# Performance work log

Measured on AMD Instinct MI355X. Metric: run time of the kernel, lower is better.

The kernel has to match this reference:

```python
import jax, jax.numpy as jnp
import numpy as np

N, S, C, E = 32768, 32768, 1024, 16384   # nodes, subgraph-node entries, clusters (=B*P), coarsen edges
F, D, B, P, NC = 64, 64, 16, 64, 10      # feat dim, hidden, graphs, patches per graph, classes


def setup_inputs():
    key = jax.random.key(0)
    ks = list(jax.random.split(key, 24))
    p = lambda k, shp: jax.random.normal(k, shp, dtype=jnp.float32) * 0.05
    z = lambda n: jnp.zeros((n,), jnp.float32)
    return {
        "x": jax.random.normal(ks[0], (N, F), dtype=jnp.float32),
        "subgraphs_nodes_mapper": jax.random.randint(ks[1], (S,), 0, N, dtype=jnp.int32),
        "subgraphs_batch": jnp.sort(jax.random.randint(ks[2], (S,), 0, C, dtype=jnp.int32)),
        "subgraphs_batch_row": jax.random.randint(ks[3], (E,), 0, C, dtype=jnp.int32),
        "subgraphs_batch_col": jax.random.randint(ks[4], (E,), 0, C, dtype=jnp.int32),
        "coarsen_edge_attr": jax.random.uniform(ks[5], (E,), dtype=jnp.float32),
        "W_in1": p(ks[6], (F, D)), "b_in1": z(D),
        "W_in2": p(ks[7], (D, D)), "b_in2": z(D),
        "W_pre1": p(ks[8], (D, D)), "b_pre1": z(D),
        "W_pre2": p(ks[9], (D, D)), "b_pre2": z(D),
        "W_post1": p(ks[10], (D, D)), "b_post1": z(D),
        "W_post2": p(ks[11], (D, D)), "b_post2": z(D),
        "W_K": p(ks[12], (D, D)), "b_K": z(D),
        "W_V": p(ks[13], (D, D)), "b_V": z(D),
        "alpha_beta": jax.random.normal(ks[14], (2,), dtype=jnp.float32),
        "W_c1": p(ks[15], (D, D // 2)), "b_c1": z(D // 2),
        "W_c2": p(ks[16], (D // 2, NC)), "b_c2": z(NC),
    }


def reference(x, subgraphs_nodes_mapper, subgraphs_batch, subgraphs_batch_row,
              subgraphs_batch_col, coarsen_edge_attr,
              W_in1, b_in1, W_in2, b_in2, W_pre1, b_pre1, W_pre2, b_pre2,
              W_post1, b_post1, W_post2, b_post2, W_K, b_K, W_V, b_V,
              alpha_beta, W_c1, b_c1, W_c2, b_c2):
    seg_sum = lambda v, idx: jax.ops.segment_sum(v, idx, num_segments=C)
    # input transform MLP (use_gnn=False path)
    h = jax.nn.relu(x @ W_in1 + b_in1)
    h = jax.nn.relu(h @ W_in2 + b_in2)
    sx = h[subgraphs_nodes_mapper]                        # [S, D] irregular gather
    b = subgraphs_batch
    row, col = subgraphs_batch_row, subgraphs_batch_col
    # bincount-based symmetric degree normalization of coarsened edge weights
    deg = seg_sum(coarsen_edge_attr, row)                 # [C]
    dinv = jnp.where(deg > 0, deg ** -0.5, 0.0)
    ea = dinv[row] * coarsen_edge_attr * dinv[col]        # [E]
    # Q path: pre-deepset -> scatter sum -> post-deepset
    Q = jax.nn.relu(sx @ W_pre1 + b_pre1) @ W_pre2 + b_pre2
    Qs = seg_sum(Q, b)
    Qs = jax.nn.relu(Qs @ W_post1 + b_post1) @ W_post2 + b_post2  # [C, D]
    # K / V paths
    K = sx @ W_K + b_K                                    # [S, D]
    cnt = jnp.maximum(seg_sum(jnp.ones((S,), sx.dtype), b), 1.0)
    Ks = seg_sum(K, b) / cnt[:, None]                     # scatter-mean [C, D]
    V = sx @ W_V + b_V                                    # [S, D]
    # relu kernelization
    Qk, Kk, Ksk = jax.nn.relu(Qs), jax.nn.relu(K), jax.nn.relu(Ks)
    ab = jax.nn.softmax(alpha_beta)
    sa, sb = ab[0] ** -0.5, ab[1] ** -0.5
    ck = jnp.concatenate([sa * Ksk[b], sb * Kk], axis=-1)   # [S, 2D]
    cq = jnp.concatenate([sa * Qk, sb * Qk], axis=-1)       # [C, 2D] (diffQ=False)
    ck_s = seg_sum(ck, b)                                   # [C, 2D]
    M = ck[:, :, None] * V[:, None, :]                      # [S, 2D, D] per-entry outer product
    Ms = seg_sum(M, b)                                      # [C, 2D, D]
    # Double_Level_MessageProp / KeyProp on coarsened graph: out[c] = sum_e ea_e * x[row_e] at col_e
    Ms = seg_sum(ea[:, None, None] * Ms[row], col)
    ck_s = seg_sum(ea[:, None] * ck_s[row], col)
    H = jnp.einsum('ci,cij->cj', cq, Ms)                    # [C, D]
    den = jnp.sum(cq * ck_s, axis=-1, keepdims=True) + 1e-6
    out = H / den                                           # [C, D]
    g = out.reshape(B, P, D).mean(axis=1)                   # mean readout over patches
    logits = jax.nn.relu(g @ W_c1 + b_c1) @ W_c2 + b_c2     # [B, NC]
    return logits
```

## Files before the change

### kernel.cpp

```cpp
#include <hip/hip_runtime.h>
#include <math.h>

constexpr int NN = 32768;
constexpr int SS = 32768;
constexpr int CC = 1024;
constexpr int EE = 16384;
constexpr int BB = 16;
constexpr int PP = 64;
constexpr int NC = 10;

__device__ __forceinline__ float rdlane(float v, int l) {
    return __int_as_float(__builtin_amdgcn_readlane(__float_as_int(v), l));
}

__global__ __launch_bounds__(256) void k_zero(float* __restrict__ zbase)
{
    int i = blockIdx.x * 256 + threadIdx.x;
    *(float4*)(zbase + (size_t)i * 4) = make_float4(0.f, 0.f, 0.f, 0.f);
}

#define TS 68

__device__ __forceinline__ void gemm64(const float* A, const float* W,
                                       const float* __restrict__ bias,
                                       int r0, int c0, float acc[4][4])
{
#pragma unroll
    for (int dc = 0; dc < 4; ++dc) {
        float bv = bias[c0 + dc];
        acc[0][dc] = bv; acc[1][dc] = bv; acc[2][dc] = bv; acc[3][dc] = bv;
    }
#pragma unroll 16
    for (int k = 0; k < 64; ++k) {
        float4 av = *(const float4*)(A + k * TS + r0);
        float4 wv = *(const float4*)(W + k * TS + c0);
        acc[0][0] = fmaf(av.x, wv.x, acc[0][0]); acc[0][1] = fmaf(av.x, wv.y, acc[0][1]);
        acc[0][2] = fmaf(av.x, wv.z, acc[0][2]); acc[0][3] = fmaf(av.x, wv.w, acc[0][3]);
        acc[1][0] = fmaf(av.y, wv.x, acc[1][0]); acc[1][1] = fmaf(av.y, wv.y, acc[1][1]);
        acc[1][2] = fmaf(av.y, wv.z, acc[1][2]); acc[1][3] = fmaf(av.y, wv.w, acc[1][3]);
        acc[2][0] = fmaf(av.z, wv.x, acc[2][0]); acc[2][1] = fmaf(av.z, wv.y, acc[2][1]);
        acc[2][2] = fmaf(av.z, wv.z, acc[2][2]); acc[2][3] = fmaf(av.z, wv.w, acc[2][3]);
        acc[3][0] = fmaf(av.w, wv.x, acc[3][0]); acc[3][1] = fmaf(av.w, wv.y, acc[3][1]);
        acc[3][2] = fmaf(av.w, wv.z, acc[3][2]); acc[3][3] = fmaf(av.w, wv.w, acc[3][3]);
    }
}

__device__ __forceinline__ void gemm64x2(const float* A, const float* W1_, const float* W2_,
                                         const float* __restrict__ bias1,
                                         const float* __restrict__ bias2,
                                         int r0, int c0, float acc1[4][4], float acc2[4][4])
{
#pragma unroll
    for (int dc = 0; dc < 4; ++dc) {
        float bv1 = bias1[c0 + dc], bv2 = bias2[c0 + dc];
#pragma unroll
        for (int dr = 0; dr < 4; ++dr) { acc1[dr][dc] = bv1; acc2[dr][dc] = bv2; }
    }
#pragma unroll 8
    for (int k = 0; k < 64; ++k) {
        float4 av = *(const float4*)(A + k * TS + r0);
        float4 w1 = *(const float4*)(W1_ + k * TS + c0);
        float4 w2 = *(const float4*)(W2_ + k * TS + c0);
        float ar[4] = {av.x, av.y, av.z, av.w};
        float u1[4] = {w1.x, w1.y, w1.z, w1.w};
        float u2[4] = {w2.x, w2.y, w2.z, w2.w};
#pragma unroll
        for (int dr = 0; dr < 4; ++dr)
#pragma unroll
            for (int dc = 0; dc < 4; ++dc) {
                acc1[dr][dc] = fmaf(ar[dr], u1[dc], acc1[dr][dc]);
                acc2[dr][dc] = fmaf(ar[dr], u2[dc], acc2[dr][dc]);
            }
    }
}

__device__ __forceinline__ void stageW(float* dst, const float* __restrict__ src, int tid)
{
#pragma unroll
    for (int t = 0; t < 16; ++t) {
        int idx = tid + t * 256;
        dst[(idx >> 6) * TS + (idx & 63)] = src[idx];
    }
}

__device__ __forceinline__ void outT_relu(float* dst, int r0, int c0, float acc[4][4])
{
#pragma unroll
    for (int dc = 0; dc < 4; ++dc) {
        *(float4*)(dst + (c0 + dc) * TS + r0) =
            make_float4(fmaxf(acc[0][dc], 0.f), fmaxf(acc[1][dc], 0.f),
                        fmaxf(acc[2][dc], 0.f), fmaxf(acc[3][dc], 0.f));
    }
}

__device__ __forceinline__ void outG2(float* __restrict__ dst, size_t rowbase, int ld,
                                      int off, int r0, int c0, float acc[4][4], bool dorelu)
{
#pragma unroll
    for (int dr = 0; dr < 4; ++dr) {
        float4 v = make_float4(acc[dr][0], acc[dr][1], acc[dr][2], acc[dr][3]);
        if (dorelu) {
            v.x = fmaxf(v.x, 0.f); v.y = fmaxf(v.y, 0.f);
            v.z = fmaxf(v.z, 0.f); v.w = fmaxf(v.w, 0.f);
        }
        *(float4*)(dst + (rowbase + r0 + dr) * ld + off + c0) = v;
    }
}

__global__ __launch_bounds__(256) void k_node(
    const float* __restrict__ x,
    const float* __restrict__ W1, const float* __restrict__ b1,
    const float* __restrict__ W2, const float* __restrict__ b2,
    const float* __restrict__ Wp1, const float* __restrict__ bp1,
    const float* __restrict__ WK, const float* __restrict__ bK,
    const float* __restrict__ WV, const float* __restrict__ bV,
    float* __restrict__ u, float* __restrict__ KV)
{
    __shared__ __align__(16) float bufA[64 * TS];
    __shared__ __align__(16) float bufB[64 * TS];
    __shared__ __align__(16) float wlds[64 * TS];
    int tid = threadIdx.x;
    int tx = tid & 15, ty = tid >> 4;
    int r0 = ty * 4, c0 = tx * 4;
    size_t rowbase = (size_t)blockIdx.x * 64;
    const float* xb = x + rowbase * 64;
#pragma unroll
    for (int t = 0; t < 16; ++t) {
        int idx = tid + t * 256;
        bufA[(idx & 63) * TS + (idx >> 6)] = xb[idx];
    }
    stageW(wlds, W1, tid);
    __syncthreads();
    float acc[4][4];
    gemm64(bufA, wlds, b1, r0, c0, acc);
    outT_relu(bufB, r0, c0, acc);
    __syncthreads();
    stageW(wlds, W2, tid);
    __syncthreads();
    gemm64(bufB, wlds, b2, r0, c0, acc);
    outT_relu(bufA, r0, c0, acc);
    __syncthreads();
    stageW(wlds, Wp1, tid);
    __syncthreads();
    gemm64(bufA, wlds, bp1, r0, c0, acc);
    outG2(u, rowbase, 64, 0, r0, c0, acc, true);
    __syncthreads();
    stageW(wlds, WK, tid);
    stageW(bufB, WV, tid);
    __syncthreads();
    float accV[4][4];
    gemm64x2(bufA, wlds, bufB, bK, bV, r0, c0, acc, accV);
    outG2(KV, rowbase, 128, 0, r0, c0, acc, false);
    outG2(KV, rowbase, 128, 64, r0, c0, accV, false);
}

__global__ void k_prep1(const int* __restrict__ row, const float* __restrict__ attr,
                        float* __restrict__ deg, int* __restrict__ rowcnt, int E)
{
    int e = blockIdx.x * 256 + threadIdx.x;
    if (e < E) {
        int r = row[e];
        atomicAdd(&deg[r], attr[e]);
        atomicAdd(&rowcnt[r], 1);
    }
}

__global__ __launch_bounds__(1024) void k_scan(
    const int* __restrict__ rowcnt, int* __restrict__ rowptr, int* __restrict__ rowfill,
    const int* __restrict__ batch, int* __restrict__ segoff)
{
    __shared__ int buf[1024];
    int tid = threadIdx.x;
    int v = rowcnt[tid];
    buf[tid] = v;
    __syncthreads();
    for (int off = 1; off < 1024; off <<= 1) {
        int t = (tid >= off) ? buf[tid - off] : 0;
        __syncthreads();
        buf[tid] += t;
        __syncthreads();
    }
    int incl = buf[tid];
    if (tid == 0) rowptr[0] = 0;
    rowptr[tid + 1] = incl;
    rowfill[tid] = incl - v;
    int lo = 0, hi = SS;
    while (lo < hi) { int mid = (lo + hi) >> 1; if (batch[mid] < tid) lo = mid + 1; else hi = mid; }
    segoff[tid] = lo;
    if (tid == 0) segoff[CC] = SS;
}

__global__ void k_prep2(const int* __restrict__ row, const int* __restrict__ col,
                        const float* __restrict__ attr, const float* __restrict__ deg,
                        int* __restrict__ rowfill, int* __restrict__ colS,
                        float* __restrict__ eawS, int E)
{
    int e = blockIdx.x * 256 + threadIdx.x;
    if (e < E) {
        int r = row[e], c = col[e];
        float dr = deg[r], dc = deg[c];
        float ir = dr > 0.f ? 1.f / sqrtf(dr) : 0.f;
        float ic = dc > 0.f ? 1.f / sqrtf(dc) : 0.f;
        int pos = atomicAdd(&rowfill[r], 1);
        colS[pos] = c;
        eawS[pos] = ir * attr[e] * ic;
    }
}

#define KSTR 72

__global__ __launch_bounds__(256, 4) void k_msb(
    const float* __restrict__ u, const float* __restrict__ KV,
    const int* __restrict__ mapper, const int* __restrict__ segoff,
    const float* __restrict__ Wp2, const float* __restrict__ bp2,
    const float* __restrict__ Wpo1, const float* __restrict__ bpo1,
    const float* __restrict__ Wpo2, const float* __restrict__ bpo2,
    float* __restrict__ Msb, float* __restrict__ Qk, float* __restrict__ Ksk,
    float* __restrict__ Krsum, float* __restrict__ Vsum, float* __restrict__ Lf)
{
    __shared__ __align__(16) float Kr[32 * KSTR];
    __shared__ __align__(16) float Vb[32 * KSTR];
    __shared__ int map_lds[32];
    __shared__ float sums[256];
    __shared__ float redu0[64], redu1[64], redu2[64];
    int c = blockIdx.x;
    int tid = threadIdx.x, j = tid & 63, g = tid >> 6;
    int tx = tid & 15, ty = tid >> 4;
    int r0 = ty * 4, c0 = tx * 4;
    int s0 = segoff[c], s1 = segoff[c + 1];
    sums[tid] = 0.f;
    float acc[4][4];
#pragma unroll
    for (int a = 0; a < 4; ++a)
#pragma unroll
        for (int b = 0; b < 4; ++b) acc[a][b] = 0.f;
    float qs = 0.f, ks = 0.f, krs = 0.f, vs = 0.f;
    __syncthreads();
    for (int sb = s0; sb < s1; sb += 32) {
        int clen = min(32, s1 - sb);
        __syncthreads();
        if (tid < clen) map_lds[tid] = mapper[sb + tid];
        __syncthreads();
        for (int p = tid; p < clen * 32; p += 256) {
            int e = p >> 5, q = p & 31;
            int m = map_lds[e];
            float4 v = *(const float4*)(KV + (size_t)m * 128 + q * 4);
            float* dst = (q < 16) ? &Kr[e * KSTR + q * 4] : &Vb[e * KSTR + (q - 16) * 4];
            *(float4*)dst = v;
        }
        __syncthreads();
#pragma unroll 4
        for (int s = 0; s < clen; ++s) {
            float4 a4 = *(const float4*)(&Kr[s * KSTR + r0]);
            float4 b4 = *(const float4*)(&Vb[s * KSTR + c0]);
            float ar0 = fmaxf(a4.x, 0.f), ar1 = fmaxf(a4.y, 0.f);
            float ar2 = fmaxf(a4.z, 0.f), ar3 = fmaxf(a4.w, 0.f);
            acc[0][0] = fmaf(ar0, b4.x, acc[0][0]); acc[0][1] = fmaf(ar0, b4.y, acc[0][1]);
            acc[0][2] = fmaf(ar0, b4.z, acc[0][2]); acc[0][3] = fmaf(ar0, b4.w, acc[0][3]);
            acc[1][0] = fmaf(ar1, b4.x, acc[1][0]); acc[1][1] = fmaf(ar1, b4.y, acc[1][1]);
            acc[1][2] = fmaf(ar1, b4.z, acc[1][2]); acc[1][3] = fmaf(ar1, b4.w, acc[1][3]);
            acc[2][0] = fmaf(ar2, b4.x, acc[2][0]); acc[2][1] = fmaf(ar2, b4.y, acc[2][1]);
            acc[2][2] = fmaf(ar2, b4.z, acc[2][2]); acc[2][3] = fmaf(ar2, b4.w, acc[2][3]);
            acc[3][0] = fmaf(ar3, b4.x, acc[3][0]); acc[3][1] = fmaf(ar3, b4.y, acc[3][1]);
            acc[3][2] = fmaf(ar3, b4.z, acc[3][2]); acc[3][3] = fmaf(ar3, b4.w, acc[3][3]);
        }
        for (int s = g; s < clen; s += 4) {
            float kv = Kr[s * KSTR + j];
            ks += kv;
            krs += fmaxf(kv, 0.f);
            vs += Vb[s * KSTR + j];
            qs += u[(size_t)map_lds[s] * 64 + j];
        }
    }
    atomicAdd(&sums[j], qs);
    atomicAdd(&sums[64 + j], ks);
    atomicAdd(&sums[128 + j], krs);
    atomicAdd(&sums[192 + j], vs);
    size_t mb = (size_t)c * 4096;
#pragma unroll
    for (int a = 0; a < 4; ++a)
        *(float4*)(Msb + mb + (size_t)(r0 + a) * 64 + c0) =
            make_float4(acc[a][0], acc[a][1], acc[a][2], acc[a][3]);
    int L = s1 - s0;
    if (tid < 64) {
        redu0[tid] = (float)L * bp2[tid];
        redu1[tid] = bpo1[tid];
        redu2[tid] = bpo2[tid];
    }
    __syncthreads();
    float qsv = sums[j];
    float Lm = (float)(L > 0 ? L : 1);
    if (g == 0) {
        Ksk[c * 64 + j] = fmaxf(sums[64 + j] / Lm, 0.f);
        Krsum[c * 64 + j] = sums[128 + j];
        Vsum[c * 64 + j] = sums[192 + j];
        if (j == 0) Lf[c] = (float)L;
    }
    float p = 0.f;
#pragma unroll
    for (int t = 0; t < 16; ++t) {
        int i = g * 16 + t;
        p = fmaf(rdlane(qsv, i), Wp2[i * 64 + j], p);
    }
    atomicAdd(&redu0[j], p);
    __syncthreads();
    float q2 = redu0[j];
    p = 0.f;
#pragma unroll
    for (int t = 0; t < 16; ++t) {
        int i = g * 16 + t;
        p = fmaf(rdlane(q2, i), Wpo1[i * 64 + j], p);
    }
    atomicAdd(&redu1[j], p);
    __syncthreads();
    float tt = fmaxf(redu1[j], 0.f);
    p = 0.f;
#pragma unroll
    for (int t = 0; t < 16; ++t) {
        int i = g * 16 + t;
        p = fmaf(rdlane(tt, i), Wpo2[i * 64 + j], p);
    }
    atomicAdd(&redu2[j], p);
    __syncthreads();
    if (tid < 64) Qk[c * 64 + tid] = fmaxf(redu2[tid], 0.f);
}

#define MSTR 68

__global__ __launch_bounds__(256, 4) void k_edges(
    const float* __restrict__ Msb, const float* __restrict__ Qk,
    const float* __restrict__ Ksk, const float* __restrict__ Krsum,
    const float* __restrict__ Vsum, const float* __restrict__ Lf,
    const float* __restrict__ eawS, const int* __restrict__ colS,
    const int* __restrict__ rowptr, const float* __restrict__ ab,
    float* __restrict__ H, float* __restrict__ den)
{
    __shared__ __align__(16) float msb[64 * MSTR];
    int r = blockIdx.x;
    int e0 = rowptr[r], e1 = rowptr[r + 1];
    if (e0 == e1) return;
    int tid = threadIdx.x, j = tid & 63, g = tid >> 6;
    size_t mb = (size_t)r * 4096;
    for (int p = tid; p < 1024; p += 256) {
        float4 v = *(const float4*)(Msb + mb + (size_t)p * 4);
        int i = p >> 4, j0 = (p & 15) * 4;
        *(float4*)(&msb[i * MSTR + j0]) = v;
    }
    float kskj = Ksk[r * 64 + j];
    float krj  = Krsum[r * 64 + j];
    float vsj  = Vsum[r * 64 + j];
    float Lr   = Lf[r];
    float a0 = ab[0], a1 = ab[1];
    float sa2 = 1.f + expf(a1 - a0);
    float sb2 = 1.f + expf(a0 - a1);
    __syncthreads();
    int idx = e0 + g;
    if (idx >= e1) return;
    int c = colS[idx];
    float w = eawS[idx];
    float qv = Qk[c * 64 + j];
    while (true) {
        int cc = c; float wc = w, qc = qv;
        int nidx = idx + 4;
        if (nidx < e1) {
            c = colS[nidx];
            w = eawS[nidx];
            qv = Qk[c * 64 + j];
        }
        float wj0 = 0.f, wj1 = 0.f, wj2 = 0.f, wj3 = 0.f;
#pragma unroll
        for (int t = 0; t < 16; ++t) {
            wj0 = fmaf(rdlane(qc, 4 * t + 0), msb[(4 * t + 0) * MSTR + j], wj0);
            wj1 = fmaf(rdlane(qc, 4 * t + 1), msb[(4 * t + 1) * MSTR + j], wj1);
            wj2 = fmaf(rdlane(qc, 4 * t + 2), msb[(4 * t + 2) * MSTR + j], wj2);
            wj3 = fmaf(rdlane(qc, 4 * t + 3), msb[(4 * t + 3) * MSTR + j], wj3);
        }
        float wjt = (wj0 + wj1) + (wj2 + wj3);
        float p1 = qc * kskj;
        float p2 = qc * krj;
#pragma unroll
        for (int o = 32; o > 0; o >>= 1) { p1 += __shfl_xor(p1, o); p2 += __shfl_xor(p2, o); }
        atomicAdd(&H[cc * 64 + j], wc * (sb2 * wjt + sa2 * p1 * vsj));
        if (j == 0) atomicAdd(&den[cc], wc * (sa2 * Lr * p1 + sb2 * p2));
        idx = nidx;
        if (idx >= e1) break;
    }
}

__global__ __launch_bounds__(64) void k_final(
    const float* __restrict__ H, const float* __restrict__ den,
    const float* __restrict__ Wc1, const float* __restrict__ bc1,
    const float* __restrict__ Wc2, const float* __restrict__ bc2,
    float* __restrict__ out)
{
    int bg = blockIdx.x;
    int j = threadIdx.x;
    float acc = 0.f;
    for (int p = 0; p < PP; ++p) {
        int c = bg * PP + p;
        acc += H[c * 64 + j] / (den[c] + 1e-6f);
    }
    float g = acc * (1.f / (float)PP);
    int m = j & 31;
    float a1 = bc1[m];
#pragma unroll
    for (int i = 0; i < 64; ++i) a1 = fmaf(rdlane(g, i), Wc1[i * 32 + m], a1);
    float c1 = fmaxf(a1, 0.f);
    int n = (j < NC) ? j : 0;
    float a2 = bc2[n];
#pragma unroll
    for (int i = 0; i < 32; ++i) a2 = fmaf(rdlane(c1, i), Wc2[i * NC + n], a2);
    if (j < NC) out[bg * NC + j] = a2;
}

extern "C" void kernel_launch(void* const* d_in, const int* in_sizes, int n_in,
                              void* d_out, int out_size, void* d_ws, size_t ws_size,
                              hipStream_t stream)
{
    const float* x      = (const float*)d_in[0];
    const int*   mapper = (const int*)d_in[1];
    const int*   batch  = (const int*)d_in[2];
    const int*   row    = (const int*)d_in[3];
    const int*   col    = (const int*)d_in[4];
    const float* attr   = (const float*)d_in[5];
    const float* W_in1  = (const float*)d_in[6];
    const float* b_in1  = (const float*)d_in[7];
    const float* W_in2  = (const float*)d_in[8];
    const float* b_in2  = (const float*)d_in[9];
    const float* W_pre1 = (const float*)d_in[10];
    const float* b_pre1 = (const float*)d_in[11];
    const float* W_pre2 = (const float*)d_in[12];
    const float* b_pre2 = (const float*)d_in[13];
    const float* W_post1= (const float*)d_in[14];
    const float* b_post1= (const float*)d_in[15];
    const float* W_post2= (const float*)d_in[16];
    const float* b_post2= (const float*)d_in[17];
    const float* W_K    = (const float*)d_in[18];
    const float* b_K    = (const float*)d_in[19];
    const float* W_V    = (const float*)d_in[20];
    const float* b_V    = (const float*)d_in[21];
    const float* alpha_beta = (const float*)d_in[22];
    const float* W_c1   = (const float*)d_in[23];
    const float* b_c1   = (const float*)d_in[24];
    const float* W_c2   = (const float*)d_in[25];
    const float* b_c2   = (const float*)d_in[26];

    float* ws = (float*)d_ws;
    float* u     = ws;
    float* KV    = u     + (size_t)NN * 64;
    float* Qk    = KV    + (size_t)NN * 128;
    float* eawS  = Qk    + (size_t)CC * 64;
    float* Msb   = eawS  + (size_t)EE;
    float* Ksk   = Msb   + (size_t)CC * 4096;
    float* Krsum = Ksk   + (size_t)CC * 64;
    float* Vsum  = Krsum + (size_t)CC * 64;
    float* Lf    = Vsum  + (size_t)CC * 64;
    float* H     = Lf    + (size_t)CC;
    float* den   = H     + (size_t)CC * 64;
    float* deg   = den   + (size_t)CC;
    int*  rowcnt = (int*)(deg + (size_t)CC);
    int*  segoff = rowcnt + CC;
    int*  rowptr = segoff + (CC + 1);
    int*  rowfill= rowptr + (CC + 1);
    int*  colS   = rowfill + CC;

    k_zero<<<67, 256, 0, stream>>>(H);
    k_prep1<<<EE / 256, 256, 0, stream>>>(row, attr, deg, rowcnt, EE);
    k_scan<<<1, 1024, 0, stream>>>(rowcnt, rowptr, rowfill, batch, segoff);
    k_prep2<<<EE / 256, 256, 0, stream>>>(row, col, attr, deg, rowfill, colS, eawS, EE);
    k_node<<<NN / 64, 256, 0, stream>>>(x, W_in1, b_in1, W_in2, b_in2,
                                        W_pre1, b_pre1, W_K, b_K, W_V, b_V, u, KV);
    k_msb<<<CC, 256, 0, stream>>>(u, KV, mapper, segoff,
                                  W_pre2, b_pre2, W_post1, b_post1,
                                  W_post2, b_post2,
                                  Msb, Qk, Ksk, Krsum, Vsum, Lf);
    k_edges<<<CC, 256, 0, stream>>>(Msb, Qk, Ksk, Krsum, Vsum, Lf, eawS, colS,
                                    rowptr, alpha_beta, H, den);
    k_final<<<BB, 64, 0, stream>>>(H, den, W_c1, b_c1, W_c2, b_c2, (float*)d_out);
}
```

Measured before the change: 105.3 us.

## Fuse graph prep into one block kernel and double-buffer weights in node MLP

Replaces the separate zero, degree/count, scan and CSR-fill kernels with a single 1024-thread kernel that keeps degrees, counts and fill counters in shared memory. The zeroing of H/den moves into k_node. k_node now prefetches the next weight matrix into registers with vectorized loads and alternates between two LDS weight buffers, which removes a barrier per layer. The aim is fewer launches and less global atomic traffic, at the cost of a serial one-block prep stage and more LDS per block in k_node, which may lower occupancy.

```diff
diff --git a/kernel.cpp b/kernel.cpp
--- a/kernel.cpp
+++ b/kernel.cpp
@@ -13,10 +13,56 @@
     return __int_as_float(__builtin_amdgcn_readlane(__float_as_int(v), l));
 }
 
-__global__ __launch_bounds__(256) void k_zero(float* __restrict__ zbase)
-{
-    int i = blockIdx.x * 256 + threadIdx.x;
-    *(float4*)(zbase + (size_t)i * 4) = make_float4(0.f, 0.f, 0.f, 0.f);
+__global__ __launch_bounds__(1024) void k_graph(
+    const int* __restrict__ row, const int* __restrict__ col,
+    const float* __restrict__ attr, const int* __restrict__ batch,
+    int* __restrict__ segoff, int* __restrict__ rowptr,
+    int* __restrict__ colS, float* __restrict__ eawS)
+{
+    __shared__ float ldeg[1024];
+    __shared__ int lcnt[1024];
+    __shared__ int lscan[1024];
+    __shared__ int lfill[1024];
+    int tid = threadIdx.x;
+    ldeg[tid] = 0.f; lcnt[tid] = 0;
+    __syncthreads();
+#pragma unroll
+    for (int i = 0; i < 16; ++i) {
+        int e = i * 1024 + tid;
+        int r = row[e];
+        atomicAdd(&ldeg[r], attr[e]);
+        atomicAdd(&lcnt[r], 1);
+    }
+    __syncthreads();
+    int v = lcnt[tid];
+    lscan[tid] = v;
+    __syncthreads();
+    for (int off = 1; off < 1024; off <<= 1) {
+        int t = (tid >= off) ? lscan[tid - off] : 0;
+        __syncthreads();
+        lscan[tid] += t;
+        __syncthreads();
+    }
+    int incl = lscan[tid];
+    if (tid == 0) rowptr[0] = 0;
+    rowptr[tid + 1] = incl;
+    lfill[tid] = incl - v;
+    int lo = 0, hi = SS;
+    while (lo < hi) { int mid = (lo + hi) >> 1; if (batch[mid] < tid) lo = mid + 1; else hi = mid; }
+    segoff[tid] = lo;
+    if (tid == 0) segoff[CC] = SS;
+    __syncthreads();
+#pragma unroll
+    for (int i = 0; i < 16; ++i) {
+        int e = i * 1024 + tid;
+        int r = row[e], c = col[e];
+        float dr = ldeg[r], dc = ldeg[c];
+        float ir = dr > 0.f ? 1.f / sqrtf(dr) : 0.f;
+        float ic = dc > 0.f ? 1.f / sqrtf(dc) : 0.f;
+        int pos = atomicAdd(&lfill[r], 1);
+        colS[pos] = c;
+        eawS[pos] = ir * attr[e] * ic;
+    }
 }
 
 #define TS 68
@@ -45,7 +91,7 @@
     }
 }
 
-__device__ __forceinline__ void gemm64x2(const float* A, const float* W1_, const float* W2_,
+__device__ __forceinline__ void gemm64x2(const float* A, const float* Wa, const float* Wb,
                                          const float* __restrict__ bias1,
                                          const float* __restrict__ bias2,
                                          int r0, int c0, float acc1[4][4], float acc2[4][4])
@@ -59,8 +105,8 @@
 #pragma unroll 8
     for (int k = 0; k < 64; ++k) {
         float4 av = *(const float4*)(A + k * TS + r0);
-        float4 w1 = *(const float4*)(W1_ + k * TS + c0);
-        float4 w2 = *(const float4*)(W2_ + k * TS + c0);
+        float4 w1 = *(const float4*)(Wa + k * TS + c0);
+        float4 w2 = *(const float4*)(Wb + k * TS + c0);
         float ar[4] = {av.x, av.y, av.z, av.w};
         float u1[4] = {w1.x, w1.y, w1.z, w1.w};
         float u2[4] = {w2.x, w2.y, w2.z, w2.w};
@@ -74,13 +120,38 @@
     }
 }
 
-__device__ __forceinline__ void stageW(float* dst, const float* __restrict__ src, int tid)
-{
-#pragma unroll
-    for (int t = 0; t < 16; ++t) {
-        int idx = tid + t * 256;
-        dst[(idx >> 6) * TS + (idx & 63)] = src[idx];
-    }
+__device__ __forceinline__ void writeW(float* dst, int tid,
+                                       float4 a, float4 b, float4 c, float4 d)
+{
+    int colq = (tid & 15) * 4;
+    int rb = tid >> 4;
+    *(float4*)(dst + (rb     ) * TS + colq) = a;
+    *(float4*)(dst + (rb + 16) * TS + colq) = b;
+    *(float4*)(dst + (rb + 32) * TS + colq) = c;
+    *(float4*)(dst + (rb + 48) * TS + colq) = d;
+}
+
+__device__ __forceinline__ void writeXT(float* dst, int tid,
+                                        float4 a, float4 b, float4 c, float4 d)
+{
+    int rb = (tid * 4) & 63;
+    int cb = tid >> 4;
+    dst[(rb + 0) * TS + cb     ] = a.x;
+    dst[(rb + 1) * TS + cb     ] = a.y;
+    dst[(rb + 2) * TS + cb     ] = a.z;
+    dst[(rb + 3) * TS + cb     ] = a.w;
+    dst[(rb + 0) * TS + cb + 16] = b.x;
+    dst[(rb + 1) * TS + cb + 16] = b.y;
+    dst[(rb + 2) * TS + cb + 16] = b.z;
+    dst[(rb + 3) * TS + cb + 16] = b.w;
+    dst[(rb + 0) * TS + cb + 32] = c.x;
+    dst[(rb + 1) * TS + cb + 32] = c.y;
+    dst[(rb + 2) * TS + cb + 32] = c.z;
+    dst[(rb + 3) * TS + cb + 32] = c.w;
+    dst[(rb + 0) * TS + cb + 48] = d.x;
+    dst[(rb + 1) * TS + cb + 48] = d.y;
+    dst[(rb + 2) * TS + cb + 48] = d.z;
+    dst[(rb + 3) * TS + cb + 48] = d.w;
 }
 
 __device__ __forceinline__ void outT_relu(float* dst, int r0, int c0, float acc[4][4])
@@ -107,104 +178,72 @@
     }
 }
 
-__global__ __launch_bounds__(256) void k_node(
+__global__ __launch_bounds__(256, 2) void k_node(
     const float* __restrict__ x,
     const float* __restrict__ W1, const float* __restrict__ b1,
     const float* __restrict__ W2, const float* __restrict__ b2,
     const float* __restrict__ Wp1, const float* __restrict__ bp1,
     const float* __restrict__ WK, const float* __restrict__ bK,
     const float* __restrict__ WV, const float* __restrict__ bV,
-    float* __restrict__ u, float* __restrict__ KV)
+    float* __restrict__ u, float* __restrict__ KV, float* __restrict__ zbase)
 {
     __shared__ __align__(16) float bufA[64 * TS];
     __shared__ __align__(16) float bufB[64 * TS];
-    __shared__ __align__(16) float wlds[64 * TS];
+    __shared__ __align__(16) float w0[64 * TS];
+    __shared__ __align__(16) float w1[64 * TS];
     int tid = threadIdx.x;
+    if (tid < 33) {
+        int i = blockIdx.x * 33 + tid;
+        if (i < 16640) ((float4*)zbase)[i] = make_float4(0.f, 0.f, 0.f, 0.f);
+    }
     int tx = tid & 15, ty = tid >> 4;
     int r0 = ty * 4, c0 = tx * 4;
     size_t rowbase = (size_t)blockIdx.x * 64;
     const float* xb = x + rowbase * 64;
-#pragma unroll
-    for (int t = 0; t < 16; ++t) {
-        int idx = tid + t * 256;
-        bufA[(idx & 63) * TS + (idx >> 6)] = xb[idx];
-    }
-    stageW(wlds, W1, tid);
-    __syncthreads();
-    float acc[4][4];
-    gemm64(bufA, wlds, b1, r0, c0, acc);
+    float4 a0 = ((const float4*)W1)[tid];
+    float4 a1 = ((const float4*)W1)[tid + 256];
+    float4 a2 = ((const float4*)W1)[tid + 512];
+    float4 a3 = ((const float4*)W1)[tid + 768];
+    float4 x0 = ((const float4*)xb)[tid];
+    float4 x1 = ((const float4*)xb)[tid + 256];
+    float4 x2 = ((const float4*)xb)[tid + 512];
+    float4 x3 = ((const float4*)xb)[tid + 768];
+    writeW(w0, tid, a0, a1, a2, a3);
+    writeXT(bufA, tid, x0, x1, x2, x3);
+    __syncthreads();
+    float acc[4][4], accV[4][4];
+    a0 = ((const float4*)W2)[tid];
+    a1 = ((const float4*)W2)[tid + 256];
+    a2 = ((const float4*)W2)[tid + 512];
+    a3 = ((const float4*)W2)[tid + 768];
+    gemm64(bufA, w0, b1, r0, c0, acc);
     outT_relu(bufB, r0, c0, acc);
-    __syncthreads();
-    stageW(wlds, W2, tid);
-    __syncthreads();
-    gemm64(bufB, wlds, b2, r0, c0, acc);
+    writeW(w1, tid, a0, a1, a2, a3);
+    __syncthreads();
+    a0 = ((const float4*)Wp1)[tid];
+    a1 = ((const float4*)Wp1)[tid + 256];
+    a2 = ((const float4*)Wp1)[tid + 512];
+    a3 = ((const float4*)Wp1)[tid + 768];
+    gemm64(bufB, w1, b2, r0, c0, acc);
     outT_relu(bufA, r0, c0, acc);
-    __syncthreads();
-    stageW(wlds, Wp1, tid);
-    __syncthreads();
-    gemm64(bufA, wlds, bp1, r0, c0, acc);
+    writeW(w0, tid, a0, a1, a2, a3);
+    __syncthreads();
+    a0 = ((const float4*)WK)[tid];
+    a1 = ((const float4*)WK)[tid + 256];
+    a2 = ((const float4*)WK)[tid + 512];
+    a3 = ((const float4*)WK)[tid + 768];
+    float4 v0 = ((const float4*)WV)[tid];
+    float4 v1 = ((const float4*)WV)[tid + 256];
+    float4 v2 = ((const float4*)WV)[tid + 512];
+    float4 v3 = ((const float4*)WV)[tid + 768];
+    gemm64(bufA, w0, bp1, r0, c0, acc);
     outG2(u, rowbase, 64, 0, r0, c0, acc, true);
-    __syncthreads();
-    stageW(wlds, WK, tid);
-    stageW(bufB, WV, tid);
-    __syncthreads();
-    float accV[4][4];
-    gemm64x2(bufA, wlds, bufB, bK, bV, r0, c0, acc, accV);
+    writeW(w1, tid, a0, a1, a2, a3);
+    writeW(bufB, tid, v0, v1, v2, v3);
+    __syncthreads();
+    gemm64x2(bufA, w1, bufB, bK, bV, r0, c0, acc, accV);
     outG2(KV, rowbase, 128, 0, r0, c0, acc, false);
     outG2(KV, rowbase, 128, 64, r0, c0, accV, false);
-}
-
-__global__ void k_prep1(const int* __restrict__ row, const float* __restrict__ attr,
-                        float* __restrict__ deg, int* __restrict__ rowcnt, int E)
-{
-    int e = blockIdx.x * 256 + threadIdx.x;
-    if (e < E) {
-        int r = row[e];
-        atomicAdd(&deg[r], attr[e]);
-        atomicAdd(&rowcnt[r], 1);
-    }
-}
-
-__global__ __launch_bounds__(1024) void k_scan(
-    const int* __restrict__ rowcnt, int* __restrict__ rowptr, int* __restrict__ rowfill,
-    const int* __restrict__ batch, int* __restrict__ segoff)
-{
-    __shared__ int buf[1024];
-    int tid = threadIdx.x;
-    int v = rowcnt[tid];
-    buf[tid] = v;
-    __syncthreads();
-    for (int off = 1; off < 1024; off <<= 1) {
-        int t = (tid >= off) ? buf[tid - off] : 0;
-        __syncthreads();
-        buf[tid] += t;
-        __syncthreads();
-    }
-    int incl = buf[tid];
-    if (tid == 0) rowptr[0] = 0;
-    rowptr[tid + 1] = incl;
-    rowfill[tid] = incl - v;
-    int lo = 0, hi = SS;
-    while (lo < hi) { int mid = (lo + hi) >> 1; if (batch[mid] < tid) lo = mid + 1; else hi = mid; }
-    segoff[tid] = lo;
-    if (tid == 0) segoff[CC] = SS;
-}
-
-__global__ void k_prep2(const int* __restrict__ row, const int* __restrict__ col,
-                        const float* __restrict__ attr, const float* __restrict__ deg,
-                        int* __restrict__ rowfill, int* __restrict__ colS,
-                        float* __restrict__ eawS, int E)
-{
-    int e = blockIdx.x * 256 + threadIdx.x;
-    if (e < E) {
-        int r = row[e], c = col[e];
-        float dr = deg[r], dc = deg[c];
-        float ir = dr > 0.f ? 1.f / sqrtf(dr) : 0.f;
-        float ic = dc > 0.f ? 1.f / sqrtf(dc) : 0.f;
-        int pos = atomicAdd(&rowfill[r], 1);
-        colS[pos] = c;
-        eawS[pos] = ir * attr[e] * ic;
-    }
 }
 
 #define KSTR 72
@@ -457,19 +496,13 @@
     float* Lf    = Vsum  + (size_t)CC * 64;
     float* H     = Lf    + (size_t)CC;
     float* den   = H     + (size_t)CC * 64;
-    float* deg   = den   + (size_t)CC;
-    int*  rowcnt = (int*)(deg + (size_t)CC);
-    int*  segoff = rowcnt + CC;
+    int*  segoff = (int*)(den + (size_t)CC);
     int*  rowptr = segoff + (CC + 1);
-    int*  rowfill= rowptr + (CC + 1);
-    int*  colS   = rowfill + CC;
-
-    k_zero<<<67, 256, 0, stream>>>(H);
-    k_prep1<<<EE / 256, 256, 0, stream>>>(row, attr, deg, rowcnt, EE);
-    k_scan<<<1, 1024, 0, stream>>>(rowcnt, rowptr, rowfill, batch, segoff);
-    k_prep2<<<EE / 256, 256, 0, stream>>>(row, col, attr, deg, rowfill, colS, eawS, EE);
+    int*  colS   = rowptr + (CC + 1);
+
+    k_graph<<<1, 1024, 0, stream>>>(row, col, attr, batch, segoff, rowptr, colS, eawS);
     k_node<<<NN / 64, 256, 0, stream>>>(x, W_in1, b_in1, W_in2, b_in2,
-                                        W_pre1, b_pre1, W_K, b_K, W_V, b_V, u, KV);
+                                        W_pre1, b_pre1, W_K, b_K, W_V, b_V, u, KV, H);
     k_msb<<<CC, 256, 0, stream>>>(u, KV, mapper, segoff,
                                   W_pre2, b_pre2, W_post1, b_post1,
                                   W_post2, b_post2,
```

Result: slower. 135.3 us (+28.5%).
